# Optimization experiments

Hardware: AMD Instinct MI355X
Metric: run time of the kernel (lower is better)

## Reference

```python
import jax, jax.numpy as jnp
import numpy as np

N_NODES = 50000
N_EDGES = 800000
HIDDEN = 128
CONTEXT = 128


def setup_inputs() -> dict:
    key = jax.random.key(0)
    ks = jax.random.split(key, 8)
    s = 1.0 / np.sqrt(HIDDEN)
    return {
        "x": jax.random.normal(ks[0], (N_NODES, HIDDEN), jnp.float32),
        "edge_index": jax.random.randint(ks[1], (2, N_EDGES), 0, N_NODES, jnp.int64),
        "W_le": jax.random.normal(ks[2], (HIDDEN, 1), jnp.float32) * s,
        "b_le": jnp.zeros((1,), jnp.float32),
        "W1": jax.random.normal(ks[3], (HIDDEN, HIDDEN), jnp.float32) * s,
        "b1": jnp.zeros((HIDDEN,), jnp.float32),
        "W2": jax.random.normal(ks[4], (HIDDEN, CONTEXT), jnp.float32) * s,
        "b2": jnp.zeros((CONTEXT,), jnp.float32),
    }


def reference(x, edge_index, W_le, b_le, W1, b1, W2, b2):
    N = x.shape[0]
    src, dst = edge_index[0], edge_index[1]
    ar = jnp.arange(N)

    # leader election logits [N]
    logits = (x @ W_le + b_le)[:, 0]

    # extended edges with self loops (every destination segment non-empty)
    ext_src = jnp.concatenate([src, ar])
    ext_dst = jnp.concatenate([dst, ar])

    # scatter_max of source logits onto destinations; recover winning SOURCE node index
    val = logits[ext_src]                                   # [E+N]
    seg_max = jax.ops.segment_max(val, ext_dst, num_segments=N)  # [N]
    winner = jnp.where(val == seg_max[ext_dst], ext_src, -1)
    leader_idx = jax.ops.segment_max(winner, ext_dst, num_segments=N)  # [N] int
    is_leader = ar == leader_idx                            # [N] bool

    # scatter_mean of neighbor features onto destinations
    nsum = jax.ops.segment_sum(x[src], dst, num_segments=N)            # [N, H]
    cnt = jax.ops.segment_sum(jnp.ones((src.shape[0],), x.dtype), dst, num_segments=N)
    nmean = nsum / jnp.maximum(cnt, 1.0)[:, None]

    # squad report MLP (exact GELU, matching torch nn.GELU default)
    h = jax.nn.gelu(nmean @ W1 + b1, approximate=False)
    reports = h @ W2 + b2                                   # [N, C]
    all_reports = jnp.where(is_leader[:, None], reports, 0.0)

    # each node reads its leader's report
    squad_context = all_reports[leader_idx]                 # [N, C]
    return squad_context
```

## Files before the change

### kernel.cpp

```cpp
#include <hip/hip_runtime.h>
#include <stdint.h>

constexpr int NN  = 50000;
constexpr int NE  = 800000;
constexpr int H   = 128;
constexpr int CAP = 48;
constexpr int RB  = 8;

__device__ __forceinline__ uint32_t f32key(float f) {
  uint32_t b = __float_as_uint(f);
  return (b & 0x80000000u) ? ~b : (b | 0x80000000u);
}

__global__ void k_logits(const float* __restrict__ x,
                         const float* __restrict__ Wle, const float* __restrict__ ble,
                         float* __restrict__ logits, unsigned long long* __restrict__ lkey,
                         int* __restrict__ cnt, int* __restrict__ nsl) {
  int gid  = blockIdx.x * blockDim.x + threadIdx.x;
  int wave = gid >> 6, lane = threadIdx.x & 63;
  if (gid == 0) *nsl = 0;
  if (wave >= NN) return;
  const float* xr = x + (size_t)wave * H;
  float v = xr[lane] * Wle[lane] + xr[lane + 64] * Wle[lane + 64];
  for (int off = 32; off > 0; off >>= 1) v += __shfl_xor(v, off, 64);
  if (lane == 0) {
    float lg = v + ble[0];
    logits[wave] = lg;
    lkey[wave] = ((unsigned long long)f32key(lg) << 32) | (unsigned long long)(uint32_t)wave;
    cnt[wave] = 0;
  }
}

__global__ void k_elect(const int* __restrict__ esrc, const int* __restrict__ edst,
                        const float* __restrict__ logits, unsigned long long* __restrict__ lkey) {
  int e = blockIdx.x * blockDim.x + threadIdx.x;
  if (e >= NE) return;
  int s = __builtin_nontemporal_load(&esrc[e]);
  int d = __builtin_nontemporal_load(&edst[e]);
  unsigned long long key =
      ((unsigned long long)f32key(logits[s]) << 32) | (unsigned long long)(uint32_t)s;
  atomicMax(&lkey[d], key);
}

__global__ void k_place(const int* __restrict__ esrc, const int* __restrict__ edst,
                        const unsigned long long* __restrict__ lkey,
                        int* __restrict__ cnt, int* __restrict__ bucket,
                        int* __restrict__ slist, int* __restrict__ nsl) {
  const int* __restrict__ leader_lo = (const int*)lkey;
  int t = blockIdx.x * blockDim.x + threadIdx.x;
  if (t < NN) {
    if (leader_lo[2 * t] == t) {
      int p = atomicAdd(nsl, 1);
      slist[p] = t;
    }
  }
  if (t >= NE) return;
  int d = __builtin_nontemporal_load(&edst[t]);
  if (leader_lo[2 * d] != d) return;
  int s = esrc[t];
  int slot = atomicAdd(&cnt[d], 1);
  if (slot < CAP) bucket[(size_t)d * CAP + slot] = s;
}

__global__ void __launch_bounds__(128) k_gather(
    const int* __restrict__ slist, const int* __restrict__ nsl,
    const int* __restrict__ cnt, const int* __restrict__ bucket,
    const float* __restrict__ x, float* __restrict__ out) {
  int b = blockIdx.x;
  if (b >= *nsl) return;
  int node = slist[b];
  int c = cnt[node];
  int cc = min(c, CAP);
  __shared__ int ss[CAP];
  int j = threadIdx.x;
  if (j < cc) ss[j] = bucket[(size_t)node * CAP + j];
  __syncthreads();
  double a0 = 0.0, a1 = 0.0;
  int e = 0;
  for (; e + 1 < cc; e += 2) {
    a0 += (double)x[(size_t)ss[e] * H + j];
    a1 += (double)x[(size_t)ss[e + 1] * H + j];
  }
  if (e < cc) a0 += (double)x[(size_t)ss[e] * H + j];
  float rc = 1.0f / (float)max(c, 1);
  out[(size_t)node * H + j] = (float)(a0 + a1) * rc;
}

__global__ void __launch_bounds__(128) k_mlp8(
    const int* __restrict__ slist, const int* __restrict__ nsl,
    const float* __restrict__ W1, const float* __restrict__ b1,
    const float* __restrict__ W2, const float* __restrict__ b2,
    float* __restrict__ out) {
  int base = blockIdx.x * RB;
  int ns = *nsl;
  if (base >= ns) return;
  int v = min(RB, ns - base);
  __shared__ float sm[RB][H];
  __shared__ int nodes[RB];
  int j = threadIdx.x;
  if (j < RB) nodes[j] = (j < v) ? slist[base + j] : 0;
  __syncthreads();
#pragma unroll
  for (int r = 0; r < RB; ++r)
    if (r < v) sm[r][j] = out[(size_t)nodes[r] * H + j];
  __syncthreads();
  float acc[RB];
#pragma unroll
  for (int r = 0; r < RB; ++r) acc[r] = b1[j];
  for (int k = 0; k < H; ++k) {
    float w = W1[k * H + j];
#pragma unroll
    for (int r = 0; r < RB; ++r) acc[r] = fmaf(sm[r][k], w, acc[r]);
  }
  __syncthreads();
#pragma unroll
  for (int r = 0; r < RB; ++r)
    sm[r][j] = 0.5f * acc[r] * (1.0f + erff(acc[r] * 0.70710678118654752f));
  __syncthreads();
#pragma unroll
  for (int r = 0; r < RB; ++r) acc[r] = b2[j];
  for (int k = 0; k < H; ++k) {
    float w = W2[k * H + j];
#pragma unroll
    for (int r = 0; r < RB; ++r) acc[r] = fmaf(sm[r][k], w, acc[r]);
  }
#pragma unroll
  for (int r = 0; r < RB; ++r)
    if (r < v) out[(size_t)nodes[r] * H + j] = acc[r];
}

__global__ void k_out(const unsigned long long* __restrict__ lkey,
                      float* __restrict__ out) {
  const int* __restrict__ leader_lo = (const int*)lkey;
  int g = blockIdx.x * blockDim.x + threadIdx.x;
  int i = g >> 5, q = g & 31;
  if (i >= NN) return;
  int L = leader_lo[2 * i];
  if (L == i) return;
  float4 v = make_float4(0.f, 0.f, 0.f, 0.f);
  if (leader_lo[2 * L] == L)
    v = *(const float4*)(out + (size_t)L * H + q * 4);
  *(float4*)(out + (size_t)i * H + q * 4) = v;
}

extern "C" void kernel_launch(void* const* d_in, const int* in_sizes, int n_in,
                              void* d_out, int out_size, void* d_ws, size_t ws_size,
                              hipStream_t stream) {
  (void)in_sizes; (void)n_in; (void)out_size; (void)ws_size;
  const float* x   = (const float*)d_in[0];
  const int* ei    = (const int*)d_in[1];
  const float* Wle = (const float*)d_in[2];
  const float* ble = (const float*)d_in[3];
  const float* W1  = (const float*)d_in[4];
  const float* b1  = (const float*)d_in[5];
  const float* W2  = (const float*)d_in[6];
  const float* b2  = (const float*)d_in[7];
  float* out       = (float*)d_out;

  char* ws = (char*)d_ws;
  unsigned long long* lkey = (unsigned long long*)ws;
  float* logits = (float*)(ws + 400000);
  int*   cnt    = (int*)  (ws + 600000);
  int*   slist  = (int*)  (ws + 800000);
  int*   nsl    = (int*)  (ws + 1000000);
  int*   bucket = (int*)  (ws + 1000256);

  const int* esrc = ei;
  const int* edst = ei + NE;

  k_logits<<<(NN * 64 + 255) / 256, 256, 0, stream>>>(x, Wle, ble, logits, lkey, cnt, nsl);
  k_elect<<<(NE + 255) / 256, 256, 0, stream>>>(esrc, edst, logits, lkey);
  k_place<<<(NE + 255) / 256, 256, 0, stream>>>(esrc, edst, lkey, cnt, bucket, slist, nsl);
  k_gather<<<NN, 128, 0, stream>>>(slist, nsl, cnt, bucket, x, out);
  k_mlp8<<<(NN + RB - 1) / RB, 128, 0, stream>>>(slist, nsl, W1, b1, W2, b2, out);
  k_out<<<(NN * 32 + 255) / 256, 256, 0, stream>>>(lkey, out);
}
```

Baseline: 107.9 us.

## Fuse neighbor-mean gather into leader MLP kernel with two half-blocks

Merges the per-leader gather kernel and the MLP kernel into one 256-thread kernel. Each block handles 8 leaders: each 128-thread half gathers neighbor sums for alternating rows, then computes the MLP for 4 rows. This removes one launch and the write-then-reread of the mean row through global memory. Output stores in the report and broadcast kernels become nontemporal. The cost is more shared memory per block, and each thread now does the serial gather for several rows.

```diff
diff --git a/kernel.cpp b/kernel.cpp
--- a/kernel.cpp
+++ b/kernel.cpp
@@ -62,32 +62,10 @@
   if (slot < CAP) bucket[(size_t)d * CAP + slot] = s;
 }
 
-__global__ void __launch_bounds__(128) k_gather(
+__global__ void __launch_bounds__(256) k_report(
     const int* __restrict__ slist, const int* __restrict__ nsl,
     const int* __restrict__ cnt, const int* __restrict__ bucket,
-    const float* __restrict__ x, float* __restrict__ out) {
-  int b = blockIdx.x;
-  if (b >= *nsl) return;
-  int node = slist[b];
-  int c = cnt[node];
-  int cc = min(c, CAP);
-  __shared__ int ss[CAP];
-  int j = threadIdx.x;
-  if (j < cc) ss[j] = bucket[(size_t)node * CAP + j];
-  __syncthreads();
-  double a0 = 0.0, a1 = 0.0;
-  int e = 0;
-  for (; e + 1 < cc; e += 2) {
-    a0 += (double)x[(size_t)ss[e] * H + j];
-    a1 += (double)x[(size_t)ss[e + 1] * H + j];
-  }
-  if (e < cc) a0 += (double)x[(size_t)ss[e] * H + j];
-  float rc = 1.0f / (float)max(c, 1);
-  out[(size_t)node * H + j] = (float)(a0 + a1) * rc;
-}
-
-__global__ void __launch_bounds__(128) k_mlp8(
-    const int* __restrict__ slist, const int* __restrict__ nsl,
+    const float* __restrict__ x,
     const float* __restrict__ W1, const float* __restrict__ b1,
     const float* __restrict__ W2, const float* __restrict__ b2,
     float* __restrict__ out) {
@@ -95,38 +73,71 @@
   int ns = *nsl;
   if (base >= ns) return;
   int v = min(RB, ns - base);
+
   __shared__ float sm[RB][H];
-  __shared__ int nodes[RB];
-  int j = threadIdx.x;
-  if (j < RB) nodes[j] = (j < v) ? slist[base + j] : 0;
+  __shared__ float hm[RB][H];
+  __shared__ int   ss[RB][CAP];
+  __shared__ int   nodes[RB];
+  __shared__ int   craw[RB];
+
+  int tid = threadIdx.x;
+  int j = tid & 127, half = tid >> 7;
+
+  if (tid < RB) {
+    int node = slist[base + min(tid, v - 1)];
+    nodes[tid] = node;
+    craw[tid] = cnt[node];
+  }
   __syncthreads();
+  for (int r = half; r < v; r += 2) {
+    int cc = min(craw[r], CAP);
+    if (j < cc) ss[r][j] = bucket[(size_t)nodes[r] * CAP + j];
+  }
+  __syncthreads();
+  for (int rp = 0; rp < RB / 2; ++rp) {
+    int r = 2 * rp + half;
+    if (r >= v) break;
+    int c = craw[r], cc = min(c, CAP);
+    double a0 = 0.0, a1 = 0.0;
+    int e = 0;
+    for (; e + 1 < cc; e += 2) {
+      a0 += (double)x[(size_t)ss[r][e] * H + j];
+      a1 += (double)x[(size_t)ss[r][e + 1] * H + j];
+    }
+    if (e < cc) a0 += (double)x[(size_t)ss[r][e] * H + j];
+    sm[r][j] = (float)(a0 + a1) * (1.0f / (float)max(c, 1));
+  }
+  __syncthreads();
+
+  float acc[RB / 2];
 #pragma unroll
-  for (int r = 0; r < RB; ++r)
-    if (r < v) sm[r][j] = out[(size_t)nodes[r] * H + j];
-  __syncthreads();
-  float acc[RB];
-#pragma unroll
-  for (int r = 0; r < RB; ++r) acc[r] = b1[j];
+  for (int rr = 0; rr < RB / 2; ++rr) acc[rr] = b1[j];
   for (int k = 0; k < H; ++k) {
     float w = W1[k * H + j];
 #pragma unroll
-    for (int r = 0; r < RB; ++r) acc[r] = fmaf(sm[r][k], w, acc[r]);
+    for (int rr = 0; rr < RB / 2; ++rr)
+      acc[rr] = fmaf(sm[half * (RB / 2) + rr][k], w, acc[rr]);
   }
+#pragma unroll
+  for (int rr = 0; rr < RB / 2; ++rr)
+    hm[half * (RB / 2) + rr][j] =
+        0.5f * acc[rr] * (1.0f + erff(acc[rr] * 0.70710678118654752f));
   __syncthreads();
+
 #pragma unroll
-  for (int r = 0; r < RB; ++r)
-    sm[r][j] = 0.5f * acc[r] * (1.0f + erff(acc[r] * 0.70710678118654752f));
-  __syncthreads();
-#pragma unroll
-  for (int r = 0; r < RB; ++r) acc[r] = b2[j];
+  for (int rr = 0; rr < RB / 2; ++rr) acc[rr] = b2[j];
   for (int k = 0; k < H; ++k) {
     float w = W2[k * H + j];
 #pragma unroll
-    for (int r = 0; r < RB; ++r) acc[r] = fmaf(sm[r][k], w, acc[r]);
+    for (int rr = 0; rr < RB / 2; ++rr)
+      acc[rr] = fmaf(hm[half * (RB / 2) + rr][k], w, acc[rr]);
   }
 #pragma unroll
-  for (int r = 0; r < RB; ++r)
-    if (r < v) out[(size_t)nodes[r] * H + j] = acc[r];
+  for (int rr = 0; rr < RB / 2; ++rr) {
+    int r = half * (RB / 2) + rr;
+    if (r < v)
+      __builtin_nontemporal_store(acc[rr], &out[(size_t)nodes[r] * H + j]);
+  }
 }
 
 __global__ void k_out(const unsigned long long* __restrict__ lkey,
@@ -140,7 +151,11 @@
   float4 v = make_float4(0.f, 0.f, 0.f, 0.f);
   if (leader_lo[2 * L] == L)
     v = *(const float4*)(out + (size_t)L * H + q * 4);
-  *(float4*)(out + (size_t)i * H + q * 4) = v;
+  float* o = out + (size_t)i * H + q * 4;
+  __builtin_nontemporal_store(v.x, o + 0);
+  __builtin_nontemporal_store(v.y, o + 1);
+  __builtin_nontemporal_store(v.z, o + 2);
+  __builtin_nontemporal_store(v.w, o + 3);
 }
 
 extern "C" void kernel_launch(void* const* d_in, const int* in_sizes, int n_in,
@@ -171,7 +186,7 @@
   k_logits<<<(NN * 64 + 255) / 256, 256, 0, stream>>>(x, Wle, ble, logits, lkey, cnt, nsl);
   k_elect<<<(NE + 255) / 256, 256, 0, stream>>>(esrc, edst, logits, lkey);
   k_place<<<(NE + 255) / 256, 256, 0, stream>>>(esrc, edst, lkey, cnt, bucket, slist, nsl);
-  k_gather<<<NN, 128, 0, stream>>>(slist, nsl, cnt, bucket, x, out);
-  k_mlp8<<<(NN + RB - 1) / RB, 128, 0, stream>>>(slist, nsl, W1, b1, W2, b2, out);
+  k_report<<<(NN + RB - 1) / RB, 256, 0, stream>>>(slist, nsl, cnt, bucket, x,
+                                                   W1, b1, W2, b2, out);
   k_out<<<(NN * 32 + 255) / 256, 256, 0, stream>>>(lkey, out);
 }
```

Measured after the change: 99.73 us. -7.6%, faster.
